# Kernel optimization log

Hardware: AMD Instinct MI355X
Metric: run time of the kernel (lower is better)

## Reference

```python
import jax, jax.numpy as jnp
import numpy as np

N_ENTITIES = 100000
N_RELATIONS = 1000
D = 100   # embedding_size
K = 4     # tensor slices
B = 4096  # batch


def setup_inputs() -> dict:
    key = jax.random.key(0)
    k1, k2, k3, k4, k5, k6, k7, k8 = jax.random.split(key, 8)
    return {
        "heads": jax.random.randint(k1, (B,), 0, N_ENTITIES),
        "tails": jax.random.randint(k2, (B,), 0, N_ENTITIES),
        "relations": jax.random.randint(k3, (B,), 0, N_RELATIONS),
        # parameters, matching tf.random_uniform(0, 1)
        "entity_embedding": jax.random.uniform(k4, (N_ENTITIES, D), dtype=jnp.float32),
        "W": jax.random.uniform(k5, (N_RELATIONS, K, D, D), dtype=jnp.float32),
        "V": jax.random.uniform(k6, (N_RELATIONS, K, 2 * D), dtype=jnp.float32),
        "Bp": jax.random.uniform(k7, (N_RELATIONS, K), dtype=jnpp_f32 if False else jnp.float32),
        "U": jax.random.uniform(k8, (N_RELATIONS, K), dtype=jnp.float32),
    }


def reference(heads, tails, relations, entity_embedding, W, V, Bp, U):
    # gathers
    e1 = entity_embedding[heads]          # [B, D]
    e2 = entity_embedding[tails]          # [B, D]
    w = W[relations]                      # [B, K, D, D]
    v = V[relations]                      # [B, K, 2D]
    b = Bp[relations]                     # [B, K]
    u = U[relations]                      # [B, K]

    # g_a = v @ [e1; e2]
    e12 = jnp.concatenate([e1, e2], axis=1)           # [B, 2D]
    g_a = jnp.einsum('bkm,bm->bk', v, e12)            # [B, K]
    # g_b = e1^T W_k e2 (bilinear tensor product)
    g_b = jnp.einsum('bd,bkde,be->bk', e1, w, e2)     # [B, K]

    score = jnp.einsum('bk,bk->b', u, jnp.tanh(g_a + g_b + b))  # [B]
    pred = jax.nn.sigmoid(score)
    return pred
```

## Files before the change

kernel.cpp:

```cpp
#include <hip/hip_runtime.h>
#include <math.h>

#define D 100
#define K 4
#define NREL 1000
#define CH 8
#define NT 512
#define MAXB 64

__global__ __launch_bounds__(NT) void ntn_fused(
    const int* __restrict__ heads, const int* __restrict__ tails,
    const int* __restrict__ rels,
    const float* __restrict__ E, const float* __restrict__ W,
    const float* __restrict__ V, const float* __restrict__ Bp,
    const float* __restrict__ U, float* __restrict__ out, int B)
{
    const int r    = blockIdx.x;
    const int tid  = threadIdx.x;
    const int lane = tid & 63;
    const int w    = tid >> 6;
    const int k    = w & 3;
    const int half = w >> 2;
    const int dsub = lane / 25;
    const int c    = lane % 25;
    const bool active = (lane < 50);

    __shared__ int   bb[MAXB];
    __shared__ int   cntS;
    __shared__ float e12[CH][2 * D];
    __shared__ float red[8][CH];

    if (tid == 0) cntS = 0;
    __syncthreads();
    for (int b = tid; b < B; b += NT) {
        if (rels[b] == r) {
            int p = atomicAdd(&cntS, 1);
            if (p < MAXB) bb[p] = b;
        }
    }
    __syncthreads();
    const int n = min(cntS, MAXB);
    if (n == 0) return;

    const float* Wk = W + ((size_t)r * K + k) * D * D;
    const float* Vr = V + (size_t)r * K * 2 * D;

    for (int base = 0; base < n; base += CH) {
        const int m = min(CH, n - base);
        __syncthreads();
        for (int idx = tid; idx < CH * 2 * D; idx += NT) {
            const int it = idx / (2 * D), j = idx % (2 * D);
            float val = 0.f;
            if (it < m) {
                const int b = bb[base + it];
                const int ent = (j < D) ? heads[b] : tails[b];
                val = E[(size_t)ent * D + (j < D ? j : j - D)];
            }
            e12[it][j] = val;
        }
        __syncthreads();

        float4 e2r[CH];
        #pragma unroll
        for (int it = 0; it < CH; ++it)
            e2r[it] = active ? *(const float4*)&e12[it][D + c * 4]
                             : make_float4(0.f, 0.f, 0.f, 0.f);

        float acc[CH];
        #pragma unroll
        for (int it = 0; it < CH; ++it) acc[it] = 0.f;

        if (active) {
            #pragma unroll 5
            for (int dp = 0; dp < 25; ++dp) {
                const int d = half * 50 + dp * 2 + dsub;
                const float4 wv = *(const float4*)&Wk[d * D + c * 4];
                #pragma unroll
                for (int it = 0; it < CH; ++it) {
                    acc[it] += (wv.x * e2r[it].x + wv.y * e2r[it].y
                              + wv.z * e2r[it].z + wv.w * e2r[it].w) * e12[it][d];
                }
            }
        }
        if (half == 0) {
            for (int j = lane; j < 2 * D; j += 64) {
                const float vv = Vr[k * 2 * D + j];
                #pragma unroll
                for (int it = 0; it < CH; ++it) acc[it] += vv * e12[it][j];
            }
        }
        #pragma unroll
        for (int it = 0; it < CH; ++it) {
            float s = acc[it];
            #pragma unroll
            for (int off = 32; off > 0; off >>= 1) s += __shfl_down(s, off, 64);
            if (lane == 0) red[w][it] = s;
        }
        __syncthreads();
        if (tid < m) {
            float score = 0.f;
            #pragma unroll
            for (int kk = 0; kk < K; ++kk) {
                const float g = red[kk][tid] + red[4 + kk][tid] + Bp[r * K + kk];
                score += U[r * K + kk] * tanhf(g);
            }
            out[bb[base + tid]] = 1.f / (1.f + expf(-score));
        }
    }
}

extern "C" void kernel_launch(void* const* d_in, const int* in_sizes, int n_in,
                              void* d_out, int out_size, void* d_ws, size_t ws_size,
                              hipStream_t stream) {
    const int*   heads = (const int*)d_in[0];
    const int*   tails = (const int*)d_in[1];
    const int*   rels  = (const int*)d_in[2];
    const float* E     = (const float*)d_in[3];
    const float* W     = (const float*)d_in[4];
    const float* V     = (const float*)d_in[5];
    const float* Bp    = (const float*)d_in[6];
    const float* U     = (const float*)d_in[7];
    float* out = (float*)d_out;

    const int B = in_sizes[0];
    ntn_fused<<<NREL, NT, 0, stream>>>(heads, tails, rels, E, W, V, Bp, U, out, B);
}
```

Measured before the change: 57.77 us.

## Split NTN kernel per (relation, slice) block with separate sigmoid epilogue

The grid goes from one 512-thread block per relation to one 256-thread block per (relation, slice) pair, so each block streams a single W_k slice. Each block writes u_k*tanh(g_k) partials to workspace, and a second small kernel sums the four partials and applies the sigmoid. The aim is more blocks and more parallel memory streams over W. In exchange, each of the four blocks per relation rescans the relation array and regathers the embeddings, and there is an extra kernel launch plus a workspace round trip.

```diff
diff --git a/kernel.cpp b/kernel.cpp
--- a/kernel.cpp
+++ b/kernel.cpp
@@ -5,22 +5,21 @@
 #define K 4
 #define NREL 1000
 #define CH 8
-#define NT 512
+#define NT 256
 #define MAXB 64
 
-__global__ __launch_bounds__(NT) void ntn_fused(
+__global__ __launch_bounds__(NT) void ntn_partial(
     const int* __restrict__ heads, const int* __restrict__ tails,
     const int* __restrict__ rels,
     const float* __restrict__ E, const float* __restrict__ W,
     const float* __restrict__ V, const float* __restrict__ Bp,
-    const float* __restrict__ U, float* __restrict__ out, int B)
+    const float* __restrict__ U, float* __restrict__ part, int B)
 {
-    const int r    = blockIdx.x;
+    const int r    = blockIdx.x >> 2;
+    const int k    = blockIdx.x & 3;
     const int tid  = threadIdx.x;
     const int lane = tid & 63;
     const int w    = tid >> 6;
-    const int k    = w & 3;
-    const int half = w >> 2;
     const int dsub = lane / 25;
     const int c    = lane % 25;
     const bool active = (lane < 50);
@@ -28,7 +27,7 @@
     __shared__ int   bb[MAXB];
     __shared__ int   cntS;
     __shared__ float e12[CH][2 * D];
-    __shared__ float red[8][CH];
+    __shared__ float red[4][CH];
 
     if (tid == 0) cntS = 0;
     __syncthreads();
@@ -43,7 +42,9 @@
     if (n == 0) return;
 
     const float* Wk = W + ((size_t)r * K + k) * D * D;
-    const float* Vr = V + (size_t)r * K * 2 * D;
+    const float* Vk = V + ((size_t)r * K + k) * 2 * D;
+    const float  uk = U[r * K + k];
+    const float  bk = Bp[r * K + k];
 
     for (int base = 0; base < n; base += CH) {
         const int m = min(CH, n - base);
@@ -70,10 +71,10 @@
         #pragma unroll
         for (int it = 0; it < CH; ++it) acc[it] = 0.f;
 
-        if (active) {
-            #pragma unroll 5
-            for (int dp = 0; dp < 25; ++dp) {
-                const int d = half * 50 + dp * 2 + dsub;
+        #pragma unroll
+        for (int dp = 0; dp < 13; ++dp) {
+            const int d = dp * 8 + w * 2 + dsub;
+            if (active && d < D) {
                 const float4 wv = *(const float4*)&Wk[d * D + c * 4];
                 #pragma unroll
                 for (int it = 0; it < CH; ++it) {
@@ -82,12 +83,10 @@
                 }
             }
         }
-        if (half == 0) {
-            for (int j = lane; j < 2 * D; j += 64) {
-                const float vv = Vr[k * 2 * D + j];
-                #pragma unroll
-                for (int it = 0; it < CH; ++it) acc[it] += vv * e12[it][j];
-            }
+        for (int j = tid; j < 2 * D; j += NT) {
+            const float vv = Vk[j];
+            #pragma unroll
+            for (int it = 0; it < CH; ++it) acc[it] += vv * e12[it][j];
         }
         #pragma unroll
         for (int it = 0; it < CH; ++it) {
@@ -98,14 +97,19 @@
         }
         __syncthreads();
         if (tid < m) {
-            float score = 0.f;
-            #pragma unroll
-            for (int kk = 0; kk < K; ++kk) {
-                const float g = red[kk][tid] + red[4 + kk][tid] + Bp[r * K + kk];
-                score += U[r * K + kk] * tanhf(g);
-            }
-            out[bb[base + tid]] = 1.f / (1.f + expf(-score));
+            const float g = red[0][tid] + red[1][tid] + red[2][tid] + red[3][tid] + bk;
+            part[(size_t)bb[base + tid] * 4 + k] = uk * tanhf(g);
         }
+    }
+}
+
+__global__ __launch_bounds__(256) void ntn_epilogue(const float* __restrict__ part,
+                                                    float* __restrict__ out, int B) {
+    const int b = blockIdx.x * 256 + threadIdx.x;
+    if (b < B) {
+        const float4 p = *(const float4*)&part[(size_t)b * 4];
+        const float s = (p.x + p.y) + (p.z + p.w);
+        out[b] = 1.f / (1.f + expf(-s));
     }
 }
 
@@ -123,5 +127,8 @@
     float* out = (float*)d_out;
 
     const int B = in_sizes[0];
-    ntn_fused<<<NREL, NT, 0, stream>>>(heads, tails, rels, E, W, V, Bp, U, out, B);
+    float* part = (float*)d_ws;
+
+    ntn_partial<<<NREL * K, NT, 0, stream>>>(heads, tails, rels, E, W, V, Bp, U, part, B);
+    ntn_epilogue<<<(B + 255) / 256, 256, 0, stream>>>(part, out, B);
 }
```

New measurement: 75.03 us. 1.3x slower.

## Precompute relation buckets with a counting-sort kernel instead of per-block scans

Applied to the files above, without the earlier changes.

A separate single-block kernel builds a histogram, prefix sum and bucketed index lists of batch items per relation, including head and tail ids. The main kernel then reads its slice directly, so each of the 1000 blocks no longer scans all 4096 relation ids. The per-block cap of 64 items is removed. The embedding gather now loads float4 rows with one wave per item, and the W loads are batched five at a time to expose more memory parallelism. It adds a second launch and a serial single-block grouping stage on the critical path.

```diff
diff --git a/kernel.cpp b/kernel.cpp
--- a/kernel.cpp
+++ b/kernel.cpp
@@ -6,85 +6,114 @@
 #define NREL 1000
 #define CH 8
 #define NT 512
-#define MAXB 64
 
-__global__ __launch_bounds__(NT) void ntn_fused(
-    const int* __restrict__ heads, const int* __restrict__ tails,
-    const int* __restrict__ rels,
+__global__ __launch_bounds__(1024) void k_group(
+    const int* __restrict__ rels, const int* __restrict__ heads,
+    const int* __restrict__ tails, int B,
+    int* __restrict__ start, int* __restrict__ bb,
+    int* __restrict__ bh, int* __restrict__ bt)
+{
+    __shared__ int sA[1024], sB[1024];
+    const int tid = threadIdx.x;
+    sA[tid] = 0;
+    __syncthreads();
+    for (int b = tid; b < B; b += 1024) atomicAdd(&sA[rels[b]], 1);
+    __syncthreads();
+    const int v = sA[tid];
+    int* src = sA; int* dst = sB;
+    for (int off = 1; off < 1024; off <<= 1) {
+        int x = src[tid];
+        if (tid >= off) x += src[tid - off];
+        dst[tid] = x;
+        __syncthreads();
+        int* t = src; src = dst; dst = t;
+    }
+    const int excl = src[tid] - v;
+    if (tid < NREL) start[tid] = excl;
+    if (tid == 0)   start[NREL] = B;
+    int* cur = dst;
+    cur[tid] = excl;
+    __syncthreads();
+    for (int b = tid; b < B; b += 1024) {
+        const int r = rels[b];
+        const int pos = atomicAdd(&cur[r], 1);
+        bb[pos] = b;
+        bh[pos] = heads[b];
+        bt[pos] = tails[b];
+    }
+}
+
+#define WLOAD(u) const float4 wv##u = Wg4[(bat10 + (u)*2 + dsub) * 25 + c];
+#define WFMA(u) { \
+    const int drow = gbase + bat10 + (u)*2 + dsub; \
+    _Pragma("unroll") \
+    for (int it = 0; it < CH; ++it) { \
+        acc[it] += (wv##u.x * e2r[it].x + wv##u.y * e2r[it].y \
+                  + wv##u.z * e2r[it].z + wv##u.w * e2r[it].w) * e12[it][drow]; \
+    } }
+
+__global__ __launch_bounds__(NT, 4) void ntn_main(
     const float* __restrict__ E, const float* __restrict__ W,
     const float* __restrict__ V, const float* __restrict__ Bp,
-    const float* __restrict__ U, float* __restrict__ out, int B)
+    const float* __restrict__ U, const int* __restrict__ start,
+    const int* __restrict__ bb, const int* __restrict__ bh,
+    const int* __restrict__ bt, float* __restrict__ out)
 {
-    const int r    = blockIdx.x;
+    const int r  = blockIdx.x;
+    const int cs = start[r];
+    const int n  = start[r + 1] - cs;
+    if (n <= 0) return;
+
     const int tid  = threadIdx.x;
     const int lane = tid & 63;
     const int w    = tid >> 6;
     const int k    = w & 3;
-    const int half = w >> 2;
+    const int g    = w >> 2;
     const int dsub = lane / 25;
     const int c    = lane % 25;
     const bool active = (lane < 50);
+    const int gbase = g * 50;
 
-    __shared__ int   bb[MAXB];
-    __shared__ int   cntS;
     __shared__ float e12[CH][2 * D];
     __shared__ float red[8][CH];
+    __shared__ int   ob[CH];
 
-    if (tid == 0) cntS = 0;
-    __syncthreads();
-    for (int b = tid; b < B; b += NT) {
-        if (rels[b] == r) {
-            int p = atomicAdd(&cntS, 1);
-            if (p < MAXB) bb[p] = b;
-        }
-    }
-    __syncthreads();
-    const int n = min(cntS, MAXB);
-    if (n == 0) return;
-
-    const float* Wk = W + ((size_t)r * K + k) * D * D;
-    const float* Vr = V + (size_t)r * K * 2 * D;
+    const float4* Wg4 = reinterpret_cast<const float4*>(
+        W + ((size_t)r * K + k) * D * D + (size_t)gbase * D);
+    const float*  Vk  = V + ((size_t)r * K + k) * 2 * D;
+    const float4* E4  = reinterpret_cast<const float4*>(E);
 
     for (int base = 0; base < n; base += CH) {
         const int m = min(CH, n - base);
         __syncthreads();
-        for (int idx = tid; idx < CH * 2 * D; idx += NT) {
-            const int it = idx / (2 * D), j = idx % (2 * D);
-            float val = 0.f;
-            if (it < m) {
-                const int b = bb[base + it];
-                const int ent = (j < D) ? heads[b] : tails[b];
-                val = E[(size_t)ent * D + (j < D ? j : j - D)];
-            }
-            e12[it][j] = val;
+        if (tid < m) ob[tid] = bb[cs + base + tid];
+        if (active && w < m) {
+            const int idx = cs + base + w;
+            const int ent = dsub ? bt[idx] : bh[idx];
+            *(float4*)&e12[w][dsub * D + c * 4] = E4[(size_t)ent * 25 + c];
         }
         __syncthreads();
 
         float4 e2r[CH];
         #pragma unroll
         for (int it = 0; it < CH; ++it)
-            e2r[it] = active ? *(const float4*)&e12[it][D + c * 4]
-                             : make_float4(0.f, 0.f, 0.f, 0.f);
+            e2r[it] = *(const float4*)&e12[it][D + c * 4];
 
         float acc[CH];
         #pragma unroll
         for (int it = 0; it < CH; ++it) acc[it] = 0.f;
 
         if (active) {
-            #pragma unroll 5
-            for (int dp = 0; dp < 25; ++dp) {
-                const int d = half * 50 + dp * 2 + dsub;
-                const float4 wv = *(const float4*)&Wk[d * D + c * 4];
-                #pragma unroll
-                for (int it = 0; it < CH; ++it) {
-                    acc[it] += (wv.x * e2r[it].x + wv.y * e2r[it].y
-                              + wv.z * e2r[it].z + wv.w * e2r[it].w) * e12[it][d];
-                }
+            #pragma unroll 1
+            for (int bat = 0; bat < 5; ++bat) {
+                const int bat10 = bat * 10;
+                WLOAD(0) WLOAD(1) WLOAD(2) WLOAD(3) WLOAD(4)
+                WFMA(0) WFMA(1) WFMA(2) WFMA(3) WFMA(4)
             }
         }
-        if (half == 0) {
+        if (g == 0) {
             for (int j = lane; j < 2 * D; j += 64) {
-                const float vv = Vr[k * 2 * D + j];
+                const float vv = Vk[j];
                 #pragma unroll
                 for (int it = 0; it < CH; ++it) acc[it] += vv * e12[it][j];
             }
@@ -98,13 +127,14 @@
         }
         __syncthreads();
         if (tid < m) {
+            const int rb = r * K;
             float score = 0.f;
             #pragma unroll
             for (int kk = 0; kk < K; ++kk) {
-                const float g = red[kk][tid] + red[4 + kk][tid] + Bp[r * K + kk];
-                score += U[r * K + kk] * tanhf(g);
+                const float gv = red[kk][tid] + red[kk + 4][tid] + Bp[rb + kk];
+                score += U[rb + kk] * tanhf(gv);
             }
-            out[bb[base + tid]] = 1.f / (1.f + expf(-score));
+            out[ob[tid]] = 1.f / (1.f + expf(-score));
         }
     }
 }
@@ -123,5 +153,11 @@
     float* out = (float*)d_out;
 
     const int B = in_sizes[0];
-    ntn_fused<<<NREL, NT, 0, stream>>>(heads, tails, rels, E, W, V, Bp, U, out, B);
+    int* start = (int*)d_ws;
+    int* bb    = start + 1024;
+    int* bh    = bb + B;
+    int* bt    = bh + B;
+
+    k_group<<<1, 1024, 0, stream>>>(rels, heads, tails, B, start, bb, bh, bt);
+    ntn_main<<<NREL, NT, 0, stream>>>(E, W, V, Bp, U, start, bb, bh, bt, out);
 }
```

Result: slower. 68.75 us (+19.0%).

## Split each relation across two blocks and use deterministic scan-based batch compaction

Applied to the files above, without the earlier changes.

Each relation is now handled by two 256-thread blocks that take interleaved groups of 4 batch items, instead of one 512-thread block processing chunks of 8. Within a block each wave owns a full k-slice of W rather than half of one, which removes the cross-half reduction. The atomic-based batch compaction is replaced by a wave prefix-scan over contiguous rels ranges, and the entity rows are gathered with one float4 load per lane. The goal is more blocks in flight and less per-block latency, but each W slice is now read by both blocks of a relation, so W traffic can double when a relation has more than 4 items.

```diff
diff --git a/kernel.cpp b/kernel.cpp
--- a/kernel.cpp
+++ b/kernel.cpp
@@ -4,107 +4,118 @@
 #define D 100
 #define K 4
 #define NREL 1000
-#define CH 8
-#define NT 512
+#define NT 256
 #define MAXB 64
 
-__global__ __launch_bounds__(NT) void ntn_fused(
+__global__ __launch_bounds__(NT) void ntn_all(
     const int* __restrict__ heads, const int* __restrict__ tails,
     const int* __restrict__ rels,
     const float* __restrict__ E, const float* __restrict__ W,
     const float* __restrict__ V, const float* __restrict__ Bp,
     const float* __restrict__ U, float* __restrict__ out, int B)
 {
-    const int r    = blockIdx.x;
+    const int id = blockIdx.x;
+    const int r  = (id >> 4) * 8 + (id & 7);
+    const int h  = (id >> 3) & 1;
+
     const int tid  = threadIdx.x;
     const int lane = tid & 63;
     const int w    = tid >> 6;
-    const int k    = w & 3;
-    const int half = w >> 2;
     const int dsub = lane / 25;
     const int c    = lane % 25;
     const bool active = (lane < 50);
 
-    __shared__ int   bb[MAXB];
-    __shared__ int   cntS;
-    __shared__ float e12[CH][2 * D];
-    __shared__ float red[8][CH];
+    __shared__ int   lst[MAXB];
+    __shared__ int   wtot[4];
+    __shared__ float e12[4][2 * D];
+    __shared__ float red[4][4];
 
-    if (tid == 0) cntS = 0;
+    const int per = (B + NT - 1) / NT;
+    const int b0  = tid * per;
+    int myc = 0;
+    for (int j = 0; j < per; ++j) {
+        const int b = b0 + j;
+        if (b < B && rels[b] == r) ++myc;
+    }
+    int scan = myc;
+    #pragma unroll
+    for (int off = 1; off < 64; off <<= 1) {
+        const int t = __shfl_up(scan, off, 64);
+        if (lane >= off) scan += t;
+    }
+    if (lane == 63) wtot[w] = scan;
     __syncthreads();
-    for (int b = tid; b < B; b += NT) {
-        if (rels[b] == r) {
-            int p = atomicAdd(&cntS, 1);
-            if (p < MAXB) bb[p] = b;
-        }
+    int woff = 0;
+    #pragma unroll
+    for (int ww = 0; ww < 4; ++ww) if (ww < w) woff += wtot[ww];
+    const int n_all = wtot[0] + wtot[1] + wtot[2] + wtot[3];
+    const int n = min(n_all, MAXB);
+    if (n <= h * 4) return;
+    int pos = woff + (scan - myc);
+    for (int j = 0; j < per; ++j) {
+        const int b = b0 + j;
+        if (b < B && rels[b] == r) { if (pos < MAXB) lst[pos] = b; ++pos; }
     }
-    __syncthreads();
-    const int n = min(cntS, MAXB);
-    if (n == 0) return;
 
-    const float* Wk = W + ((size_t)r * K + k) * D * D;
-    const float* Vr = V + (size_t)r * K * 2 * D;
+    const float4* Wk4 = reinterpret_cast<const float4*>(W + ((size_t)r * K + w) * D * D);
+    const float*  Vk  = V + ((size_t)r * K + w) * 2 * D;
+    const float4* E4  = reinterpret_cast<const float4*>(E);
 
-    for (int base = 0; base < n; base += CH) {
-        const int m = min(CH, n - base);
+    for (int base = h * 4; base < n; base += 8) {
+        const int m = min(4, n - base);
         __syncthreads();
-        for (int idx = tid; idx < CH * 2 * D; idx += NT) {
-            const int it = idx / (2 * D), j = idx % (2 * D);
-            float val = 0.f;
-            if (it < m) {
-                const int b = bb[base + it];
-                const int ent = (j < D) ? heads[b] : tails[b];
-                val = E[(size_t)ent * D + (j < D ? j : j - D)];
-            }
-            e12[it][j] = val;
+        if (active && w < m) {
+            const int b   = lst[base + w];
+            const int ent = dsub ? tails[b] : heads[b];
+            *(float4*)&e12[w][dsub * D + c * 4] = E4[(size_t)ent * 25 + c];
         }
         __syncthreads();
 
-        float4 e2r[CH];
-        #pragma unroll
-        for (int it = 0; it < CH; ++it)
-            e2r[it] = active ? *(const float4*)&e12[it][D + c * 4]
-                             : make_float4(0.f, 0.f, 0.f, 0.f);
+        const float4 e20 = *(const float4*)&e12[0][D + c * 4];
+        const float4 e21 = *(const float4*)&e12[1][D + c * 4];
+        const float4 e22 = *(const float4*)&e12[2][D + c * 4];
+        const float4 e23 = *(const float4*)&e12[3][D + c * 4];
 
-        float acc[CH];
-        #pragma unroll
-        for (int it = 0; it < CH; ++it) acc[it] = 0.f;
-
+        float acc0 = 0.f, acc1 = 0.f, acc2 = 0.f, acc3 = 0.f;
         if (active) {
-            #pragma unroll 5
-            for (int dp = 0; dp < 25; ++dp) {
-                const int d = half * 50 + dp * 2 + dsub;
-                const float4 wv = *(const float4*)&Wk[d * D + c * 4];
-                #pragma unroll
-                for (int it = 0; it < CH; ++it) {
-                    acc[it] += (wv.x * e2r[it].x + wv.y * e2r[it].y
-                              + wv.z * e2r[it].z + wv.w * e2r[it].w) * e12[it][d];
-                }
+            #pragma unroll 4
+            for (int rr = 0; rr < 50; ++rr) {
+                const int d = rr * 2 + dsub;
+                const float4 wv = Wk4[d * 25 + c];
+                acc0 += (wv.x * e20.x + wv.y * e20.y + wv.z * e20.z + wv.w * e20.w) * e12[0][d];
+                acc1 += (wv.x * e21.x + wv.y * e21.y + wv.z * e21.z + wv.w * e21.w) * e12[1][d];
+                acc2 += (wv.x * e22.x + wv.y * e22.y + wv.z * e22.z + wv.w * e22.w) * e12[2][d];
+                acc3 += (wv.x * e23.x + wv.y * e23.y + wv.z * e23.z + wv.w * e23.w) * e12[3][d];
             }
         }
-        if (half == 0) {
-            for (int j = lane; j < 2 * D; j += 64) {
-                const float vv = Vr[k * 2 * D + j];
-                #pragma unroll
-                for (int it = 0; it < CH; ++it) acc[it] += vv * e12[it][j];
-            }
+        for (int j = lane; j < 2 * D; j += 64) {
+            const float vv = Vk[j];
+            acc0 += vv * e12[0][j];
+            acc1 += vv * e12[1][j];
+            acc2 += vv * e12[2][j];
+            acc3 += vv * e12[3][j];
         }
         #pragma unroll
-        for (int it = 0; it < CH; ++it) {
-            float s = acc[it];
-            #pragma unroll
-            for (int off = 32; off > 0; off >>= 1) s += __shfl_down(s, off, 64);
-            if (lane == 0) red[w][it] = s;
+        for (int off = 32; off > 0; off >>= 1) {
+            acc0 += __shfl_down(acc0, off, 64);
+            acc1 += __shfl_down(acc1, off, 64);
+            acc2 += __shfl_down(acc2, off, 64);
+            acc3 += __shfl_down(acc3, off, 64);
+        }
+        if (lane == 0) {
+            red[w][0] = acc0; red[w][1] = acc1;
+            red[w][2] = acc2; red[w][3] = acc3;
         }
         __syncthreads();
         if (tid < m) {
+            const int rb = r * K;
             float score = 0.f;
             #pragma unroll
             for (int kk = 0; kk < K; ++kk) {
-                const float g = red[kk][tid] + red[4 + kk][tid] + Bp[r * K + kk];
-                score += U[r * K + kk] * tanhf(g);
+                const float gv = red[kk][tid] + Bp[rb + kk];
+                score += U[rb + kk] * tanhf(gv);
             }
-            out[bb[base + tid]] = 1.f / (1.f + expf(-score));
+            out[lst[base + tid]] = 1.f / (1.f + expf(-score));
         }
     }
 }
@@ -123,5 +134,6 @@
     float* out = (float*)d_out;
 
     const int B = in_sizes[0];
-    ntn_fused<<<NREL, NT, 0, stream>>>(heads, tails, rels, E, W, V, Bp, U, out, B);
+    const int nblk = ((NREL + 7) / 8) * 16;
+    ntn_all<<<nblk, NT, 0, stream>>>(heads, tails, rels, E, W, V, Bp, U, out, B);
 }
```

Result: slower. 89.62 us (+55.1%).
